# Optimization experiments

Measured on AMD Instinct MI355X. Metric: run time of the kernel, lower is better.

The kernel has to match this reference:

```python
import jax, jax.numpy as jnp
import numpy as np

N_NODES = 100000
N_EDGES = 600000
N_FEAT = 128
N_HID = 128
N_GRAPHS = 256


def gcn_conv(x, src, dst, W, b, n_nodes):
    # PyG GCNConv: h = x @ W; add self-loops; sym-normalize; scatter-add; + bias
    h = x @ W  # [N, H]
    loop = jnp.arange(n_nodes)
    s = jnp.concatenate([src, loop])
    d = jnp.concatenate([dst, loop])
    deg = jax.ops.segment_sum(jnp.ones_like(d, dtype=h.dtype), d, num_segments=n_nodes)
    dinv = jnp.where(deg > 0, jax.lax.rsqrt(deg), 0.0)
    norm = dinv[s] * dinv[d]  # [E+N]
    msg = h[s] * norm[:, None]  # gather + scale
    out = jax.ops.segment_sum(msg, d, num_segments=n_nodes)  # scatter-add
    return out + b


def setup_inputs() -> dict:
    key = jax.random.key(0)
    ks = jax.random.split(key, 12)
    x = jax.random.normal(ks[0], (N_NODES, N_FEAT), dtype=jnp.float32)
    edge_index = jax.random.randint(ks[1], (2, N_EDGES), 0, N_NODES, dtype=jnp.int64)
    batch = jnp.sort(jax.random.randint(ks[2], (N_NODES,), 0, N_GRAPHS, dtype=jnp.int64))
    def lin(k, fi, fo):
        s = 1.0 / np.sqrt(fi)
        return jax.random.uniform(k, (fi, fo), jnp.float32, -s, s)
    params = {
        'W1': lin(ks[3], N_FEAT, N_HID), 'b1': jnp.zeros((N_HID,), jnp.float32),
        'W2': lin(ks[4], N_HID, N_HID), 'b2': jnp.zeros((N_HID,), jnp.float32),
        'W3': lin(ks[5], N_HID, N_HID), 'b3': jnp.zeros((N_HID,), jnp.float32),
        'W4': lin(ks[6], N_HID, N_HID), 'b4': jnp.zeros((N_HID,), jnp.float32),
        'Ws1': lin(ks[7], N_HID, N_HID), 'bs1': jnp.zeros((N_HID,), jnp.float32),
        'Ws2': lin(ks[8], N_HID, 1), 'bs2': jnp.zeros((1,), jnp.float32),
    }
    return {'x': x, 'edge_index': edge_index, 'batch': batch, **params}


def reference(x, edge_index, batch, W1, b1, W2, b2, W3, b3, W4, b4, Ws1, bs1, Ws2, bs2):
    src, dst = edge_index[0], edge_index[1]
    h = x
    # 2 conv blocks = 4 GCNConv layers, each followed by ReLU
    for W, b in ((W1, b1), (W2, b2), (W3, b3), (W4, b4)):
        h = jax.nn.relu(gcn_conv(h, src, dst, W, b, N_NODES))
    # global mean pool over nodes per graph
    sums = jax.ops.segment_sum(h, batch, num_segments=N_GRAPHS)  # [G, H]
    cnt = jax.ops.segment_sum(jnp.ones((h.shape[0],), h.dtype), batch, num_segments=N_GRAPHS)
    pooled = sums / jnp.maximum(cnt, 1.0)[:, None]
    # summary MLP: Linear -> ReLU -> Linear(->1)
    out = jax.nn.relu(pooled @ Ws1 + bs1) @ Ws2 + bs2  # [G, 1]
    return out
```

## Files before the change

kernel.cpp:

```cpp
#include <hip/hip_runtime.h>

#define N_NODES 100000
#define N_EDGES 600000
#define NF 128
#define NG 256

typedef _Float16 f16;
typedef f16 half8 __attribute__((ext_vector_type(8)));
typedef f16 half4v __attribute__((ext_vector_type(4)));
typedef float float4v __attribute__((ext_vector_type(4)));


__global__ void k_count(const int* __restrict__ ei, int* __restrict__ counts) {
    int e = blockIdx.x * 256 + threadIdx.x;
    if (e < N_EDGES) atomicAdd(&counts[ei[N_EDGES + e]], 1);
}

__global__ void k_scan1(const int* __restrict__ counts, int* __restrict__ row_ptr,
                        int* __restrict__ bsums, float* __restrict__ dinv) {
    __shared__ int s[256];
    int b = blockIdx.x, t = threadIdx.x;
    int base = b * 2048 + t * 8;
    int local[8];
    int sum = 0;
#pragma unroll
    for (int q = 0; q < 8; q++) {
        int idx = base + q;
        int v = (idx < N_NODES) ? counts[idx] : 0;
        if (idx < N_NODES) dinv[idx] = 1.0f / sqrtf((float)(v + 1));
        local[q] = sum;
        sum += v;
    }
    s[t] = sum;
    __syncthreads();
    for (int off = 1; off < 256; off <<= 1) {
        int v = 0;
        if (t >= off) v = s[t - off];
        __syncthreads();
        s[t] += v;
        __syncthreads();
    }
    int excl = s[t] - sum;
#pragma unroll
    for (int q = 0; q < 8; q++) {
        int idx = base + q;
        if (idx < N_NODES) row_ptr[idx] = excl + local[q];
    }
    if (t == 255) bsums[b] = s[255];
}

__global__ void k_scan3(int* __restrict__ row_ptr, const int* __restrict__ bsums,
                        int* __restrict__ cursor) {
    __shared__ int pre;
    if (threadIdx.x == 0) {
        int g = blockIdx.x >> 3;
        int s = 0;
        for (int j = 0; j < g; j++) s += bsums[j];
        pre = s;
    }
    __syncthreads();
    int i = blockIdx.x * 256 + threadIdx.x;
    if (i < N_NODES) {
        int v = row_ptr[i] + pre;
        row_ptr[i] = v;
        cursor[i] = v;
        if (i == 0) row_ptr[N_NODES] = N_EDGES;
    }
}

__global__ void k_fill(const int* __restrict__ ei, int* __restrict__ cursor,
                       int* __restrict__ col,
                       const float* __restrict__ W1, const float* __restrict__ W2,
                       const float* __restrict__ W3, const float* __restrict__ W4,
                       f16* __restrict__ wtH) {
    int e = blockIdx.x * 256 + threadIdx.x;
    if (e < N_EDGES) {
        int d = ei[N_EDGES + e];
        int p = atomicAdd(&cursor[d], 1);
        col[p] = ei[e];
    }
    if (blockIdx.x < 256) {
        int idx = blockIdx.x * 256 + threadIdx.x;
        int layer = idx >> 14;
        int rem = idx & 16383;
        int j = rem & 7;
        int lane = (rem >> 3) & 63;
        int chunk = rem >> 9;
        int wave = chunk >> 3;
        int s = (chunk >> 1) & 3;
        int ct = chunk & 1;
        int n = wave * 32 + ct * 16 + (lane & 15);
        int k = s * 32 + (lane >> 4) * 8 + j;
        const float* W = (layer == 0) ? W1 : (layer == 1) ? W2 : (layer == 2) ? W3 : W4;
        wtH[layer * 16384 + rem] = (f16)W[k * NF + n];
    }
}


template <int XIN>
__global__ __launch_bounds__(256) void k_gemm_mfma(
    const float* __restrict__ X, const f16* __restrict__ A,
    const f16* __restrict__ WTH,
    f16* __restrict__ Z, int M) {
    __shared__ __align__(16) f16 As[64 * 136];

    const int t = threadIdx.x;
    const int row0 = blockIdx.x * 64;
    const int wave = t >> 6;
    const int lane = t & 63;
    const int nl = lane & 15;
    const int quad = lane >> 4;

    auto bofs = [&](int s, int ct) {
        return (size_t)((((wave * 8 + s * 2 + ct) * 64) + lane) << 3);
    };

    half8 cbh[2];
    cbh[0] = *(const half8*)(WTH + bofs(0, 0));
    cbh[1] = *(const half8*)(WTH + bofs(0, 1));

    if (XIN) {
#pragma unroll
        for (int q = 0; q < 8; q++) {
            int lin = t + q * 256;
            int r = lin >> 5, c4 = lin & 31;
            float4 v = make_float4(0.f, 0.f, 0.f, 0.f);
            if (row0 + r < M) v = ((const float4*)(X + (size_t)(row0 + r) * NF))[c4];
            half4v hv = {(f16)v.x, (f16)v.y, (f16)v.z, (f16)v.w};
            *(half4v*)&As[r * 136 + c4 * 4] = hv;
        }
    } else {
#pragma unroll
        for (int q = 0; q < 4; q++) {
            int lin = t + q * 256;
            int r = lin >> 4, c8 = lin & 15;
            half8 v = {};
            if (row0 + r < M) v = *(const half8*)(A + (size_t)(row0 + r) * NF + c8 * 8);
            *(half8*)&As[r * 136 + c8 * 8] = v;
        }
    }
    __syncthreads();

    float4v acc[2][4];
#pragma unroll
    for (int ct = 0; ct < 2; ct++)
#pragma unroll
        for (int rt = 0; rt < 4; rt++) acc[ct][rt] = (float4v)0.f;

#pragma unroll
    for (int s = 0; s < 4; s++) {
        half8 nbh[2];
        if (s < 3) {
            nbh[0] = *(const half8*)(WTH + bofs(s + 1, 0));
            nbh[1] = *(const half8*)(WTH + bofs(s + 1, 1));
        }
        half8 fa[4];
#pragma unroll
        for (int rt = 0; rt < 4; rt++)
            fa[rt] = *(half8*)&As[(rt * 16 + nl) * 136 + s * 32 + quad * 8];
#pragma unroll
        for (int ct = 0; ct < 2; ct++)
#pragma unroll
            for (int rt = 0; rt < 4; rt++)
                acc[ct][rt] = __builtin_amdgcn_mfma_f32_16x16x32_f16(fa[rt], cbh[ct], acc[ct][rt], 0, 0, 0);
        if (s < 3) {
            cbh[0] = nbh[0]; cbh[1] = nbh[1];
        }
    }

    __syncthreads();
#pragma unroll
    for (int ct = 0; ct < 2; ct++)
#pragma unroll
        for (int rt = 0; rt < 4; rt++)
#pragma unroll
            for (int r = 0; r < 4; r++)
                As[(rt * 16 + quad * 4 + r) * 136 + wave * 32 + ct * 16 + nl] =
                    (f16)acc[ct][rt][r];
    __syncthreads();
#pragma unroll
    for (int q = 0; q < 4; q++) {
        int lin = t + q * 256;
        int r = lin >> 4, c8 = lin & 15;
        if (row0 + r < M)
            *(half8*)(Z + (size_t)(row0 + r) * NF + c8 * 8) = *(half8*)&As[r * 136 + c8 * 8];
    }
}


#define ACHUNK 4

__global__ __launch_bounds__(256) void k_agg(const f16* __restrict__ z,
                                             const float* __restrict__ dinv,
                                             const int* __restrict__ row_ptr,
                                             const int* __restrict__ col,
                                             const float* __restrict__ bias,
                                             f16* __restrict__ h) {
    const int t = threadIdx.x;
    const int slot = t >> 4;
    const int fl = t & 15;
    const int sbase = (t & 48);
    const int n0 = (blockIdx.x * 16 + slot) * ACHUNK;
    const half8* z8 = (const half8*)z;

    float bb[8];
    {
        float4 b0 = ((const float4*)bias)[fl * 2];
        float4 b1 = ((const float4*)bias)[fl * 2 + 1];
        bb[0] = b0.x; bb[1] = b0.y; bb[2] = b0.z; bb[3] = b0.w;
        bb[4] = b1.x; bb[5] = b1.y; bb[6] = b1.z; bb[7] = b1.w;
    }

    for (int n = n0; n < n0 + ACHUNK && n < N_NODES; n++) {
        const float di = dinv[n];
        const int beg = row_ptr[n];
        const int end = row_ptr[n + 1];

        float acc[8];
        {
            half8 v = z8[(size_t)n * 16 + fl];
            float w = di * di;
#pragma unroll
            for (int j = 0; j < 8; j++) acc[j] = bb[j] + (float)v[j] * w;
        }

        for (int c = beg; c < end; c += 16) {
            int mcnt = end - c; if (mcnt > 16) mcnt = 16;
            int ce = c + fl;
            int colv = (ce < end) ? col[ce] : 0;
            float dvv = dinv[colv];

            int j = 0;
            for (; j + 1 < mcnt; j += 2) {
                int s1 = __shfl(colv, sbase + j, 64);
                float w1 = __shfl(dvv, sbase + j, 64) * di;
                int s2 = __shfl(colv, sbase + j + 1, 64);
                float w2 = __shfl(dvv, sbase + j + 1, 64) * di;
                half8 v1 = z8[(size_t)s1 * 16 + fl];
                half8 v2 = z8[(size_t)s2 * 16 + fl];
#pragma unroll
                for (int q = 0; q < 8; q++) acc[q] += (float)v1[q] * w1;
#pragma unroll
                for (int q = 0; q < 8; q++) acc[q] += (float)v2[q] * w2;
            }
            if (j < mcnt) {
                int s1 = __shfl(colv, sbase + j, 64);
                float w1 = __shfl(dvv, sbase + j, 64) * di;
                half8 v1 = z8[(size_t)s1 * 16 + fl];
#pragma unroll
                for (int q = 0; q < 8; q++) acc[q] += (float)v1[q] * w1;
            }
        }

        half8 o;
#pragma unroll
        for (int j = 0; j < 8; j++) o[j] = (f16)fmaxf(acc[j], 0.f);
        ((half8*)h)[(size_t)n * 16 + fl] = o;
    }
}


#define POOL_CHUNK 64

__global__ __launch_bounds__(128) void k_pool2(const f16* __restrict__ h,
                                               const int* __restrict__ batch,
                                               float* __restrict__ pooled) {
    int f = threadIdx.x;
    int n0 = blockIdx.x * POOL_CHUNK;
    int n1 = n0 + POOL_CHUNK;
    if (n1 > N_NODES) n1 = N_NODES;
    if (n0 >= N_NODES) return;
    int g = batch[n0];
    float acc = 0.f;
    for (int n = n0; n < n1; n++) {
        int gn = batch[n];
        if (gn != g) {
            atomicAdd(&pooled[g * NF + f], acc);
            acc = 0.f;
            g = gn;
        }
        acc += (float)h[(size_t)n * NF + f];
    }
    atomicAdd(&pooled[g * NF + f], acc);
}


__global__ void k_mlp(const float* __restrict__ pooled, const int* __restrict__ batch,
                      const float* __restrict__ Ws1, const float* __restrict__ bs1,
                      const float* __restrict__ Ws2, const float* __restrict__ bs2,
                      float* __restrict__ out) {
    __shared__ float row[NF];
    __shared__ float red[NF];
    int g = blockIdx.x, f = threadIdx.x;
    int lo = 0, hi = N_NODES;
    while (lo < hi) { int mid = (lo + hi) >> 1; if (batch[mid] < g) lo = mid + 1; else hi = mid; }
    int start = lo;
    hi = N_NODES;
    while (lo < hi) { int mid = (lo + hi) >> 1; if (batch[mid] < g + 1) lo = mid + 1; else hi = mid; }
    float cnt = (float)(lo - start);
    row[f] = pooled[g * NF + f] / fmaxf(cnt, 1.f);
    __syncthreads();
    float t = bs1[f];
    for (int k = 0; k < NF; k++) t += row[k] * Ws1[k * NF + f];
    t = fmaxf(t, 0.f);
    red[f] = t * Ws2[f];
    __syncthreads();
    for (int s = 64; s > 0; s >>= 1) {
        if (f < s) red[f] += red[f + s];
        __syncthreads();
    }
    if (f == 0) out[g] = red[0] + bs2[0];
}


extern "C" void kernel_launch(void* const* d_in, const int* in_sizes, int n_in,
                              void* d_out, int out_size, void* d_ws, size_t ws_size,
                              hipStream_t stream) {
    const float* x    = (const float*)d_in[0];
    const int*   ei   = (const int*)d_in[1];
    const int*   batch= (const int*)d_in[2];
    const float* W1 = (const float*)d_in[3];  const float* b1 = (const float*)d_in[4];
    const float* W2 = (const float*)d_in[5];  const float* b2 = (const float*)d_in[6];
    const float* W3 = (const float*)d_in[7];  const float* b3 = (const float*)d_in[8];
    const float* W4 = (const float*)d_in[9];  const float* b4 = (const float*)d_in[10];
    const float* Ws1= (const float*)d_in[11]; const float* bs1= (const float*)d_in[12];
    const float* Ws2= (const float*)d_in[13]; const float* bs2= (const float*)d_in[14];
    float* out = (float*)d_out;

    char* ws = (char*)d_ws;
    size_t off = 0;
    auto alloc = [&](size_t bytes) {
        void* p = ws + off;
        off += (bytes + 255) & ~(size_t)255;
        return p;
    };
    f16*   bufZ   = (f16*)alloc((size_t)N_NODES * NF * 2);
    f16*   bufH   = (f16*)alloc((size_t)N_NODES * NF * 2);
    f16*   wtH    = (f16*)alloc((size_t)4 * NF * NF * 2);
    int*   counts = (int*)alloc((size_t)N_NODES * 4);
    int*   row_ptr= (int*)alloc((size_t)(N_NODES + 1) * 4);
    int*   cursor = (int*)alloc((size_t)N_NODES * 4);
    int*   col    = (int*)alloc((size_t)N_EDGES * 4);
    int*   bsums  = (int*)alloc(64 * 4);
    float* dinv   = (float*)alloc((size_t)N_NODES * 4);
    float* pooled = (float*)alloc((size_t)NG * NF * 4);

    hipMemsetAsync(counts, 0, (size_t)N_NODES * 4, stream);
    hipMemsetAsync(pooled, 0, (size_t)NG * NF * 4, stream);
    k_count<<<(N_EDGES + 255) / 256, 256, 0, stream>>>(ei, counts);
    int nscan = (N_NODES + 2047) / 2048;
    k_scan1<<<nscan, 256, 0, stream>>>(counts, row_ptr, bsums, dinv);
    k_scan3<<<(N_NODES + 255) / 256, 256, 0, stream>>>(row_ptr, bsums, cursor);
    k_fill<<<(N_EDGES + 255) / 256, 256, 0, stream>>>(ei, cursor, col,
                                                      W1, W2, W3, W4, wtH);

    int gblocks = (N_NODES + 63) / 64;
    int ablocks = (N_NODES + 16 * ACHUNK - 1) / (16 * ACHUNK);
    k_gemm_mfma<1><<<gblocks, 256, 0, stream>>>(x, nullptr, wtH, bufZ, N_NODES);
    k_agg<<<ablocks, 256, 0, stream>>>(bufZ, dinv, row_ptr, col, b1, bufH);
    k_gemm_mfma<0><<<gblocks, 256, 0, stream>>>(nullptr, bufH, wtH + 16384, bufZ, N_NODES);
    k_agg<<<ablocks, 256, 0, stream>>>(bufZ, dinv, row_ptr, col, b2, bufH);
    k_gemm_mfma<0><<<gblocks, 256, 0, stream>>>(nullptr, bufH, wtH + 32768, bufZ, N_NODES);
    k_agg<<<ablocks, 256, 0, stream>>>(bufZ, dinv, row_ptr, col, b3, bufH);
    k_gemm_mfma<0><<<gblocks, 256, 0, stream>>>(nullptr, bufH, wtH + 49152, bufZ, N_NODES);
    k_agg<<<ablocks, 256, 0, stream>>>(bufZ, dinv, row_ptr, col, b4, bufH);

    int pblocks = (N_NODES + POOL_CHUNK - 1) / POOL_CHUNK;
    k_pool2<<<pblocks, 128, 0, stream>>>(bufH, batch, pooled);
    k_mlp<<<NG, 128, 0, stream>>>(pooled, batch, Ws1, bs1, Ws2, bs2, out);
}
```

Before: 382.4 us.

## Fuse neighbor aggregation with the next layer's MFMA GEMM in one kernel

```diff
diff --git a/kernel.cpp b/kernel.cpp
--- a/kernel.cpp
+++ b/kernel.cpp
@@ -256,6 +256,141 @@
 #pragma unroll
         for (int j = 0; j < 8; j++) o[j] = (f16)fmaxf(acc[j], 0.f);
         ((half8*)h)[(size_t)n * 16 + fl] = o;
+    }
+}
+
+
+__global__ __launch_bounds__(256) void k_agg_gemm(
+    const f16* __restrict__ z, const float* __restrict__ dinv,
+    const int* __restrict__ row_ptr, const int* __restrict__ col,
+    const float* __restrict__ bias,
+    const f16* __restrict__ WTH,
+    f16* __restrict__ Zout) {
+    __shared__ __align__(16) f16 As[64 * 136];
+
+    const int t = threadIdx.x;
+    const int slot = t >> 4;
+    const int fl = t & 15;
+    const int sbase = (t & 48);
+    const int n0 = (blockIdx.x * 16 + slot) * ACHUNK;
+    const half8* z8 = (const half8*)z;
+
+    float bb[8];
+    {
+        float4 b0 = ((const float4*)bias)[fl * 2];
+        float4 b1 = ((const float4*)bias)[fl * 2 + 1];
+        bb[0] = b0.x; bb[1] = b0.y; bb[2] = b0.z; bb[3] = b0.w;
+        bb[4] = b1.x; bb[5] = b1.y; bb[6] = b1.z; bb[7] = b1.w;
+    }
+
+#pragma unroll 1
+    for (int i = 0; i < ACHUNK; i++) {
+        const int n = n0 + i;
+        half8 o = {};
+        if (n < N_NODES) {
+            const float di = dinv[n];
+            const int beg = row_ptr[n];
+            const int end = row_ptr[n + 1];
+
+            float acc[8];
+            {
+                half8 v = z8[(size_t)n * 16 + fl];
+                float w = di * di;
+#pragma unroll
+                for (int j = 0; j < 8; j++) acc[j] = bb[j] + (float)v[j] * w;
+            }
+
+            for (int c = beg; c < end; c += 16) {
+                int mcnt = end - c; if (mcnt > 16) mcnt = 16;
+                int ce = c + fl;
+                int colv = (ce < end) ? col[ce] : 0;
+                float dvv = dinv[colv];
+
+                int j = 0;
+                for (; j + 1 < mcnt; j += 2) {
+                    int s1 = __shfl(colv, sbase + j, 64);
+                    float w1 = __shfl(dvv, sbase + j, 64) * di;
+                    int s2 = __shfl(colv, sbase + j + 1, 64);
+                    float w2 = __shfl(dvv, sbase + j + 1, 64) * di;
+                    half8 v1 = z8[(size_t)s1 * 16 + fl];
+                    half8 v2 = z8[(size_t)s2 * 16 + fl];
+#pragma unroll
+                    for (int q = 0; q < 8; q++) acc[q] += (float)v1[q] * w1;
+#pragma unroll
+                    for (int q = 0; q < 8; q++) acc[q] += (float)v2[q] * w2;
+                }
+                if (j < mcnt) {
+                    int s1 = __shfl(colv, sbase + j, 64);
+                    float w1 = __shfl(dvv, sbase + j, 64) * di;
+                    half8 v1 = z8[(size_t)s1 * 16 + fl];
+#pragma unroll
+                    for (int q = 0; q < 8; q++) acc[q] += (float)v1[q] * w1;
+                }
+            }
+#pragma unroll
+            for (int j = 0; j < 8; j++) o[j] = (f16)fmaxf(acc[j], 0.f);
+        }
+        *(half8*)&As[(slot * ACHUNK + i) * 136 + fl * 8] = o;
+    }
+
+    const int wave = t >> 6;
+    const int lane = t & 63;
+    const int nl = lane & 15;
+    const int quad = lane >> 4;
+    const int row0 = blockIdx.x * 64;
+
+    auto bofs = [&](int s, int ct) {
+        return (size_t)((((wave * 8 + s * 2 + ct) * 64) + lane) << 3);
+    };
+
+    half8 cbh[2];
+    cbh[0] = *(const half8*)(WTH + bofs(0, 0));
+    cbh[1] = *(const half8*)(WTH + bofs(0, 1));
+    __syncthreads();
+
+    float4v acc[2][4];
+#pragma unroll
+    for (int ct = 0; ct < 2; ct++)
+#pragma unroll
+        for (int rt = 0; rt < 4; rt++) acc[ct][rt] = (float4v)0.f;
+
+#pragma unroll
+    for (int s = 0; s < 4; s++) {
+        half8 nbh[2];
+        if (s < 3) {
+            nbh[0] = *(const half8*)(WTH + bofs(s + 1, 0));
+            nbh[1] = *(const half8*)(WTH + bofs(s + 1, 1));
+        }
+        half8 fa[4];
+#pragma unroll
+        for (int rt = 0; rt < 4; rt++)
+            fa[rt] = *(half8*)&As[(rt * 16 + nl) * 136 + s * 32 + quad * 8];
+#pragma unroll
+        for (int ct = 0; ct < 2; ct++)
+#pragma unroll
+            for (int rt = 0; rt < 4; rt++)
+                acc[ct][rt] = __builtin_amdgcn_mfma_f32_16x16x32_f16(fa[rt], cbh[ct], acc[ct][rt], 0, 0, 0);
+        if (s < 3) {
+            cbh[0] = nbh[0]; cbh[1] = nbh[1];
+        }
+    }
+
+    __syncthreads();
+#pragma unroll
+    for (int ct = 0; ct < 2; ct++)
+#pragma unroll
+        for (int rt = 0; rt < 4; rt++)
+#pragma unroll
+            for (int r = 0; r < 4; r++)
+                As[(rt * 16 + quad * 4 + r) * 136 + wave * 32 + ct * 16 + nl] =
+                    (f16)acc[ct][rt][r];
+    __syncthreads();
+#pragma unroll
+    for (int q = 0; q < 4; q++) {
+        int lin = t + q * 256;
+        int r = lin >> 4, c8 = lin & 15;
+        if (row0 + r < N_NODES)
+            *(half8*)(Zout + (size_t)(row0 + r) * NF + c8 * 8) = *(half8*)&As[r * 136 + c8 * 8];
     }
 }
 
@@ -334,8 +469,8 @@
         off += (bytes + 255) & ~(size_t)255;
         return p;
     };
-    f16*   bufZ   = (f16*)alloc((size_t)N_NODES * NF * 2);
-    f16*   bufH   = (f16*)alloc((size_t)N_NODES * NF * 2);
+    f16*   bufA   = (f16*)alloc((size_t)N_NODES * NF * 2);
+    f16*   bufB   = (f16*)alloc((size_t)N_NODES * NF * 2);
     f16*   wtH    = (f16*)alloc((size_t)4 * NF * NF * 2);
     int*   counts = (int*)alloc((size_t)N_NODES * 4);
     int*   row_ptr= (int*)alloc((size_t)(N_NODES + 1) * 4);
@@ -356,16 +491,17 @@
 
     int gblocks = (N_NODES + 63) / 64;
     int ablocks = (N_NODES + 16 * ACHUNK - 1) / (16 * ACHUNK);
-    k_gemm_mfma<1><<<gblocks, 256, 0, stream>>>(x, nullptr, wtH, bufZ, N_NODES);
-    k_agg<<<ablocks, 256, 0, stream>>>(bufZ, dinv, row_ptr, col, b1, bufH);
-    k_gemm_mfma<0><<<gblocks, 256, 0, stream>>>(nullptr, bufH, wtH + 16384, bufZ, N_NODES);
-    k_agg<<<ablocks, 256, 0, stream>>>(bufZ, dinv, row_ptr, col, b2, bufH);
-    k_gemm_mfma<0><<<gblocks, 256, 0, stream>>>(nullptr, bufH, wtH + 32768, bufZ, N_NODES);
-    k_agg<<<ablocks, 256, 0, stream>>>(bufZ, dinv, row_ptr, col, b3, bufH);
-    k_gemm_mfma<0><<<gblocks, 256, 0, stream>>>(nullptr, bufH, wtH + 49152, bufZ, N_NODES);
-    k_agg<<<ablocks, 256, 0, stream>>>(bufZ, dinv, row_ptr, col, b4, bufH);
+
+    k_gemm_mfma<1><<<gblocks, 256, 0, stream>>>(x, nullptr, wtH, bufA, N_NODES);
+    k_agg_gemm<<<gblocks, 256, 0, stream>>>(bufA, dinv, row_ptr, col, b1,
+                                            wtH + 16384, bufB);
+    k_agg_gemm<<<gblocks, 256, 0, stream>>>(bufB, dinv, row_ptr, col, b2,
+                                            wtH + 32768, bufA);
+    k_agg_gemm<<<gblocks, 256, 0, stream>>>(bufA, dinv, row_ptr, col, b3,
+                                            wtH + 49152, bufB);
+    k_agg<<<ablocks, 256, 0, stream>>>(bufB, dinv, row_ptr, col, b4, bufA);
 
     int pblocks = (N_NODES + POOL_CHUNK - 1) / POOL_CHUNK;
-    k_pool2<<<pblocks, 128, 0, stream>>>(bufH, batch, pooled);
+    k_pool2<<<pblocks, 128, 0, stream>>>(bufA, batch, pooled);
     k_mlp<<<NG, 128, 0, stream>>>(pooled, batch, Ws1, bs1, Ws2, bs2, out);
 }
```

Result: faster. 368.5 us (-3.6%).
